# Kernel optimization log

Hardware: AMD Instinct MI355X
Metric: run time of the kernel (lower is better)

Reference implementation:

```python
import jax, jax.numpy as jnp
import numpy as np

D_MODEL = 1024
N_HEADS = 16
D_HEAD = D_MODEL // N_HEADS


def setup_inputs() -> dict:
    key = jax.random.key(0)
    ks = jax.random.split(key, 11)
    B, S = 2, 2048
    scale = 1.0 / np.sqrt(D_MODEL)
    inp = {
        "query": jax.random.normal(ks[0], (B, S, D_MODEL), jnp.float32),
        "key": jax.random.normal(ks[1], (B, S, D_MODEL), jnp.float32),
        "value": jax.random.normal(ks[2], (B, S, D_MODEL), jnp.float32),
        "Wq": jax.random.normal(ks[3], (D_MODEL, D_MODEL), jnp.float32) * scale,
        "bq": jnp.zeros((D_MODEL,), jnp.float32),
        "Wk": jax.random.normal(ks[4], (D_MODEL, D_MODEL), jnp.float32) * scale,
        "bk": jnp.zeros((D_MODEL,), jnp.float32),
        "Wv": jax.random.normal(ks[5], (D_MODEL, D_MODEL), jnp.float32) * scale,
        "bv": jnp.zeros((D_MODEL,), jnp.float32),
        "Wo": jax.random.normal(ks[6], (D_MODEL, D_MODEL), jnp.float32) * scale,
        "bo": jnp.zeros((D_MODEL,), jnp.float32),
    }
    return inp


def _split_heads(x):
    B, S, _ = x.shape
    return x.reshape(B, S, N_HEADS, D_HEAD).transpose(0, 2, 1, 3)  # [B,H,S,Dh]


def reference(query, key, value, Wq, bq, Wk, bk, Wv, bv, Wo, bo):
    q = _split_heads(query @ Wq + bq)
    k = _split_heads(key @ Wk + bk)
    v = _split_heads(value @ Wv + bv)
    # scores [B,H,S,S] -- faithfully materialized as in the original
    scores = jnp.einsum("bhqd,bhkd->bhqk", q, k) / np.sqrt(D_HEAD)
    attn = jax.nn.softmax(scores, axis=-1)
    out = jnp.einsum("bhqk,bhkd->bhqd", attn, v)  # [B,H,S,Dh]
    B, H, S, Dh = out.shape
    out = out.transpose(0, 2, 1, 3).reshape(B, S, H * Dh)
    return out @ Wo + bo
```

## Files before the change

kernel.cpp:

```cpp
#include <hip/hip_runtime.h>
#include <hip/hip_bf16.h>

using bf16 = __hip_bfloat16;
typedef __bf16 bf16x8 __attribute__((ext_vector_type(8)));
typedef __bf16 bf16x2v __attribute__((ext_vector_type(2)));
typedef float f32x4 __attribute__((ext_vector_type(4)));
typedef float f32x16 __attribute__((ext_vector_type(16)));

#define SEQ 2048
#define DM  1024
#define QSCALE 0.18033688011112042f

__device__ __forceinline__ f32x4 mfma16(bf16x8 a, bf16x8 b, f32x4 c) {
  return __builtin_amdgcn_mfma_f32_16x16x32_bf16(a, b, c, 0, 0, 0);
}
__device__ __forceinline__ f32x16 mfma32(bf16x8 a, bf16x8 b, f32x16 c) {
  return __builtin_amdgcn_mfma_f32_32x32x16_bf16(a, b, c, 0, 0, 0);
}
__device__ __forceinline__ void gload16(const void* g, void* l) {
  __builtin_amdgcn_global_load_lds(
      (const __attribute__((address_space(1))) unsigned int*)g,
      (__attribute__((address_space(3))) unsigned int*)l, 16, 0, 0);
}
__device__ __forceinline__ unsigned short bfbits(float x) {
  bf16 h = __float2bfloat16(x);
  return *reinterpret_cast<unsigned short*>(&h);
}
__device__ __forceinline__ unsigned pk2(float a, float b) {
#if __has_builtin(__builtin_amdgcn_cvt_pk_bf16_f32)
  bf16x2v r = __builtin_amdgcn_cvt_pk_bf16_f32(a, b);
  return *reinterpret_cast<unsigned*>(&r);
#else
  return (unsigned)bfbits(a) | ((unsigned)bfbits(b) << 16);
#endif
}
__device__ __forceinline__ float fexp2(float x) {
#if __has_builtin(__builtin_amdgcn_exp2f)
  return __builtin_amdgcn_exp2f(x);
#else
  return exp2f(x);
#endif
}
__device__ __forceinline__ void plswap(unsigned& a, unsigned& b) {
  asm("v_permlane32_swap_b32 %0, %1" : "+v"(a), "+v"(b));
}

__global__ __launch_bounds__(256) void cast_all(const float* __restrict__ q,
                                                const float* __restrict__ k,
                                                const float* __restrict__ v,
                                                const float* __restrict__ Wq,
                                                const float* __restrict__ Wk,
                                                const float* __restrict__ Wv,
                                                const float* __restrict__ Wo,
                                                bf16* __restrict__ Lx,
                                                bf16* __restrict__ Lw,
                                                bf16* __restrict__ Lwo) {
  __shared__ float tf[64][68];
  if (blockIdx.y < 3) {
    const float* src = blockIdx.y == 0 ? q : (blockIdx.y == 1 ? k : v);
    bf16* dst = Lx + (size_t)blockIdx.y * (4096ull * 1024) + (size_t)blockIdx.x * 16384;
#pragma unroll
    for (int i = 0; i < 8; ++i) {
      int u = threadIdx.x + i * 256;
      int k32 = u >> 6, l = u & 63;
      const float* p = src + (size_t)(blockIdx.x * 16 + (l & 15)) * 1024 + k32 * 32 + (l >> 4) * 8;
      float4 a = *(const float4*)p;
      float4 b = *(const float4*)(p + 4);
      alignas(16) unsigned o[4] = {pk2(a.x, a.y), pk2(a.z, a.w), pk2(b.x, b.y), pk2(b.z, b.w)};
      *(uint4*)(dst + (size_t)u * 8) = *(const uint4*)o;
    }
    return;
  }
  const int widx = blockIdx.y - 3;
  const float* W = widx == 0 ? Wq : (widx == 1 ? Wk : (widx == 2 ? Wv : Wo));
  bf16* dst = widx < 3 ? (Lw + (size_t)widx * 1048576) : Lwo;
  const int t = threadIdx.x, bx = blockIdx.x & 15, by = blockIdx.x >> 4;
#pragma unroll
  for (int i = 0; i < 4; ++i) {
    int u = t + i * 256, r = u >> 4, c4 = u & 15;
    *(float4*)&tf[r][c4 * 4] = *(const float4*)(W + (size_t)(by * 64 + r) * 1024 + bx * 64 + c4 * 4);
  }
  __syncthreads();
#pragma unroll
  for (int i = 0; i < 2; ++i) {
    int u = t + i * 256;
    int sub = u >> 6, l = u & 63;
    int n16l = sub >> 1, k32l = sub & 1;
    int nn = n16l * 16 + (l & 15);
    int kk = k32l * 32 + (l >> 4) * 8;
    alignas(16) unsigned o[4];
#pragma unroll
    for (int p = 0; p < 4; ++p) o[p] = pk2(tf[kk + 2 * p][nn], tf[kk + 2 * p + 1][nn]);
    size_t off = ((((size_t)(bx * 4 + n16l)) * 32 + (by * 2 + k32l)) * 64 + l) * 8;
    *(uint4*)(dst + off) = *(const uint4*)o;
  }
}

__global__ __launch_bounds__(512, 2) void qkv_gemm(const bf16* __restrict__ Lw,
                                                   const bf16* __restrict__ Lx,
                                                   const float* __restrict__ bq,
                                                   const float* __restrict__ bk,
                                                   const float* __restrict__ bv,
                                                   bf16* __restrict__ Lq,
                                                   bf16* __restrict__ Lk,
                                                   bf16* __restrict__ Lv) {
  __shared__ alignas(16) bf16 At[2][16384];
  __shared__ alignas(16) bf16 Bt[2][16384];
  const int t = threadIdx.x, lane = t & 63, w = t >> 6;
  const int m16 = lane & 15, g4 = lane >> 4;
  const int bid = blockIdx.y * 16 + blockIdx.x;
  const int logical = (bid & 7) * 24 + (bid >> 3);
  const int nt = logical & 15, ym = logical >> 4;
  const int third = ym >> 2, mt = ym & 3;
  const int wm = w >> 2, wn = w & 3;
  const bf16* Wb = Lw + (size_t)third * 1048576;
  const bf16* Xb = Lx + (size_t)third * (4096ull * 1024);
  f32x4 acc[8][4] = {};

#pragma unroll
  for (int ii = 0; ii < 4; ++ii) {
    int u = w * 4 + ii;
    gload16(Wb + (((size_t)(mt * 16 + (u >> 1)) * 32 + (u & 1)) * 64 + lane) * 8, (void*)&At[0][u * 512]);
    gload16(Xb + (((size_t)(nt * 16 + (u >> 1)) * 32 + (u & 1)) * 64 + lane) * 8, (void*)&Bt[0][u * 512]);
  }

  const bf16* Ab0 = (third < 2) ? At[0] : Bt[0];
  const bf16* Bb0 = (third < 2) ? Bt[0] : At[0];

  int cur = 0;
  for (int slab = 0; slab < 16; ++slab) {
    __builtin_amdgcn_s_barrier();
    __builtin_amdgcn_sched_barrier(0);
    if (slab < 15) {
      const int nb = cur ^ 1, k2 = (slab + 1) * 2;
#pragma unroll
      for (int ii = 0; ii < 4; ++ii) {
        int u = w * 4 + ii;
        gload16(Wb + (((size_t)(mt * 16 + (u >> 1)) * 32 + k2 + (u & 1)) * 64 + lane) * 8,
                (void*)&At[nb][u * 512]);
        gload16(Xb + (((size_t)(nt * 16 + (u >> 1)) * 32 + k2 + (u & 1)) * 64 + lane) * 8,
                (void*)&Bt[nb][u * 512]);
      }
      asm volatile("s_waitcnt vmcnt(8)" ::: "memory");
    } else {
      asm volatile("s_waitcnt vmcnt(0)" ::: "memory");
    }
    __builtin_amdgcn_sched_barrier(0);
    __builtin_amdgcn_s_barrier();
    __builtin_amdgcn_sched_barrier(0);

    const bf16* Ac = Ab0 + cur * 16384;
    const bf16* Bc = Bb0 + cur * 16384;
#pragma unroll
    for (int kc = 0; kc < 2; ++kc) {
      bf16x8 bfr[4];
#pragma unroll
      for (int nj = 0; nj < 4; ++nj)
        bfr[nj] = *(const bf16x8*)&Bc[((wn * 4 + nj) * 2 + kc) * 512 + lane * 8];
#pragma unroll
      for (int mh = 0; mh < 2; ++mh) {
        bf16x8 afr[4];
#pragma unroll
        for (int i = 0; i < 4; ++i)
          afr[i] = *(const bf16x8*)&Ac[((wm * 8 + mh * 4 + i) * 2 + kc) * 512 + lane * 8];
        __builtin_amdgcn_s_setprio(1);
#pragma unroll
        for (int i = 0; i < 4; ++i)
#pragma unroll
          for (int nj = 0; nj < 4; ++nj)
            acc[mh * 4 + i][nj] = mfma16(afr[i], bfr[nj], acc[mh * 4 + i][nj]);
        __builtin_amdgcn_s_setprio(0);
      }
    }
    cur ^= 1;
  }

  if (third < 2) {
    bf16* dst = third == 0 ? Lq : Lk;
    const float* bias = third == 0 ? bq : bk;
    const float sc = third == 0 ? QSCALE : 1.0f;
#pragma unroll
    for (int mi = 0; mi < 8; ++mi) {
      int doutb = mt * 256 + wm * 128 + mi * 16 + g4 * 4;
      float4 b4 = *(const float4*)(bias + doutb);
      int hh = doutb >> 6, d32 = (doutb & 63) >> 5;
      int lhi = (doutb & 31) >> 3, half = g4 & 1;
#pragma unroll
      for (int nj = 0; nj < 4; ++nj) {
        int seq = nt * 256 + wn * 64 + nj * 16 + m16;
        int bb2 = seq >> 11, s16w = (seq & 2047) >> 4;
        size_t off = ((((size_t)(bb2 * 128 + s16w)) * 16 + hh) * 2 + d32) * 512 + (m16 + 16 * lhi) * 8 + half * 4;
        uint2 pv;
        pv.x = pk2((acc[mi][nj][0] + b4.x) * sc, (acc[mi][nj][1] + b4.y) * sc);
        pv.y = pk2((acc[mi][nj][2] + b4.z) * sc, (acc[mi][nj][3] + b4.w) * sc);
        *(uint2*)(dst + off) = pv;
      }
    }
  } else {
#pragma unroll
    for (int nj = 0; nj < 4; ++nj) {
      int dout = mt * 256 + wn * 64 + nj * 16 + m16;
      float bvv = bv[dout];
      int hh = dout >> 6, dt = (dout & 63) >> 4;
#pragma unroll
      for (int mi = 0; mi < 8; ++mi) {
        int seqb = nt * 256 + wm * 128 + mi * 16 + g4 * 4;
        int b_ = seqb >> 11, kt = (seqb & 2047) >> 6, ks32 = (seqb & 63) >> 5;
        int lhi = (seqb & 31) >> 3, half = g4 & 1;
        size_t off = (((((size_t)(b_ * 32 + kt)) * 16 + hh) * 4 + dt) * 2 + ks32) * 512 + (m16 + 16 * lhi) * 8 + half * 4;
        uint2 pv;
        pv.x = pk2(acc[mi][nj][0] + bvv, acc[mi][nj][1] + bvv);
        pv.y = pk2(acc[mi][nj][2] + bvv, acc[mi][nj][3] + bvv);
        *(uint2*)(Lv + off) = pv;
      }
    }
  }
}

__global__ __launch_bounds__(512, 4) void flash(const bf16* __restrict__ Lq,
                                                const bf16* __restrict__ Lk,
                                                const bf16* __restrict__ Lv,
                                                bf16* __restrict__ Lab) {
  __shared__ alignas(16) unsigned char smem[65536];
  bf16* const Kb = (bf16*)smem;
  bf16* const Vb = (bf16*)(smem + 32768);

  const int t = threadIdx.x, lane = t & 63, w = t >> 6;
  const int l31 = lane & 31, m16 = lane & 15, hi = lane >> 5, b4 = (lane >> 4) & 1;
  const int qw = w >> 1, g = w & 1, wg = w >> 1;
  const int bid = blockIdx.x;
  const int logical = ((bid & 7) << 6) | (bid >> 3);
  const int qt = logical & 15, h = (logical >> 4) & 15, b = logical >> 8;

  bf16x8 qf[4];
  {
    const int sQ = b * 128 + qt * 8 + qw * 2 + b4;
#pragma unroll
    for (int ks = 0; ks < 4; ++ks) {
      const int d32 = ks >> 1, g4q = (ks & 1) * 2 + hi;
      qf[ks] = *(const bf16x8*)(Lq + (((size_t)sQ * 16 + h) * 2 + d32) * 512 + (m16 + 16 * g4q) * 8);
    }
  }

  const int ss = wg >> 1, sd = wg & 1;
#pragma unroll
  for (int u = 0; u < 2; ++u) {
    const bf16* gk = Lk + ((((size_t)(b * 128 + g * 64 + u * 2 + ss)) * 16 + h) * 2 + sd) * 512 + lane * 8;
    gload16(gk, (void*)(Kb + (g * 2 + 0) * 4096 + u * 2048 + wg * 512));
    const bf16* gv = Lv + (((((size_t)(b * 32 + g * 16)) * 16 + h) * 4 + wg) * 2 + u) * 512 + lane * 8;
    gload16(gv, (void*)(Vb + (g * 2 + 0) * 4096 + u * 2048 + wg * 512));
  }

  float lrow = 0.f;
  f32x16 oacc[2] = {};
  __syncthreads();

  for (int it = 0; it < 16; ++it) {
    const int cur = it & 1;
    const bf16* const Klb = Kb + (g * 2 + cur) * 4096;
    const bf16* const Vlb = Vb + (g * 2 + cur) * 4096;
    if (it < 15) {
      const int nb = cur ^ 1;
#pragma unroll
      for (int u = 0; u < 2; ++u) {
        const int kc = (it + 1) * 2 + u;
        const bf16* gk = Lk + ((((size_t)(b * 128 + g * 64 + kc * 2 + ss)) * 16 + h) * 2 + sd) * 512 + lane * 8;
        gload16(gk, (void*)(Kb + (g * 2 + nb) * 4096 + u * 2048 + wg * 512));
        const bf16* gv = Lv + (((((size_t)(b * 32 + g * 16 + (kc >> 1))) * 16 + h) * 4 + wg) * 2 + (kc & 1)) * 512 + lane * 8;
        gload16(gv, (void*)(Vb + (g * 2 + nb) * 4096 + u * 2048 + wg * 512));
      }
    }

#pragma unroll
    for (int u = 0; u < 2; ++u) {
      const bf16* const Kl = Klb + u * 2048;
      const bf16* const Vl = Vlb + u * 2048;

      f32x16 s = {};
      __builtin_amdgcn_s_setprio(1);
#pragma unroll
      for (int ks = 0; ks < 4; ++ks) {
        const int d32 = ks >> 1, g4k = (ks & 1) * 2 + hi;
        bf16x8 kf = *(const bf16x8*)&Kl[((b4 * 2 + d32) * 64 + m16 + 16 * g4k) * 8];
        s = mfma32(kf, qf[ks], s);
      }
      __builtin_amdgcn_s_setprio(0);

      float e[16];
#pragma unroll
      for (int r = 0; r < 16; ++r) e[r] = fexp2(s[r]);
      {
        float a0 = e[0] + e[1], a1 = e[2] + e[3], a2 = e[4] + e[5], a3 = e[6] + e[7];
        float a4 = e[8] + e[9], a5 = e[10] + e[11], a6 = e[12] + e[13], a7 = e[14] + e[15];
        lrow += ((a0 + a1) + (a2 + a3)) + ((a4 + a5) + (a6 + a7));
      }
      bf16x8 bP[2];
#pragma unroll
      for (int c = 0; c < 2; ++c) {
        unsigned P0 = pk2(e[8 * c + 0], e[8 * c + 1]);
        unsigned P1 = pk2(e[8 * c + 2], e[8 * c + 3]);
        unsigned P2 = pk2(e[8 * c + 4], e[8 * c + 5]);
        unsigned P3 = pk2(e[8 * c + 6], e[8 * c + 7]);
        plswap(P0, P2);
        plswap(P1, P3);
        alignas(16) unsigned pw[4] = {P0, P1, P2, P3};
        bP[c] = *(const bf16x8*)pw;
      }

      __builtin_amdgcn_s_setprio(1);
#pragma unroll
      for (int dtile = 0; dtile < 2; ++dtile) {
        const int dt = dtile * 2 + b4;
#pragma unroll
        for (int c = 0; c < 2; ++c) {
          bf16x8 av = *(const bf16x8*)&Vl[(dt * 64 + m16 + 16 * (2 * c + hi)) * 8];
          oacc[dtile] = mfma32(av, bP[c], oacc[dtile]);
        }
      }
      __builtin_amdgcn_s_setprio(0);
    }
    __syncthreads();
  }

  lrow += __shfl_xor(lrow, 32);

  float* const Os = (float*)smem;
  float* const Ls = (float*)(smem + 32768);
  if (g == 1) {
#pragma unroll
    for (int dtile = 0; dtile < 2; ++dtile)
#pragma unroll
      for (int r = 0; r < 16; ++r)
        Os[((qw * 2 + dtile) * 16 + r) * 64 + lane] = oacc[dtile][r];
    if (hi == 0) Ls[qw * 32 + l31] = lrow;
  }
  __syncthreads();
  if (g == 0) {
    const float inv = 1.f / (lrow + Ls[qw * 32 + l31]);
    const int sQ = b * 128 + qt * 8 + qw * 2 + b4;
#pragma unroll
    for (int dtile = 0; dtile < 2; ++dtile) {
      const int k32 = h * 2 + dtile;
#pragma unroll
      for (int j = 0; j < 8; ++j) {
        const int r = 2 * j;
        float o0 = oacc[dtile][r] + Os[((qw * 2 + dtile) * 16 + r) * 64 + lane];
        float o1 = oacc[dtile][r + 1] + Os[((qw * 2 + dtile) * 16 + r + 1) * 64 + lane];
        unsigned pv = pk2(o0 * inv, o1 * inv);
        size_t off = ((size_t)sQ * 32 + k32) * 512 + (m16 + 16 * (r >> 2)) * 8 + 4 * hi + (r & 3);
        *(unsigned*)(Lab + off) = pv;
      }
    }
  }
}

__global__ __launch_bounds__(256) void out_gemm(const bf16* __restrict__ Lab,
                                                const bf16* __restrict__ Lwo,
                                                const float* __restrict__ bo,
                                                float* __restrict__ out) {
  __shared__ alignas(16) bf16 Al[2][8192];
  __shared__ alignas(16) bf16 Bl[2][4096];
  const int t = threadIdx.x, lane = t & 63, w = t >> 6;
  const int m16 = lane & 15, g4 = lane >> 4;
  const int bid = blockIdx.y * 16 + blockIdx.x;
  const int logical = (bid & 7) * 64 + (bid >> 3);
  const int nt = logical & 15, mt = logical >> 4;
  const int wm = w >> 1, wn = w & 1;
  f32x4 acc[4][2] = {};

#pragma unroll
  for (int ii = 0; ii < 4; ++ii) {
    int s = w * 4 + ii;
    gload16(Lab + (((size_t)(mt * 8 + (s >> 1))) * 32 + (s & 1)) * 512 + lane * 8, (void*)&Al[0][s * 512]);
  }
#pragma unroll
  for (int ii = 0; ii < 2; ++ii) {
    int s = w * 2 + ii;
    gload16(Lwo + (((size_t)(nt * 4 + (s >> 1))) * 32 + (s & 1)) * 512 + lane * 8, (void*)&Bl[0][s * 512]);
  }

  int cur = 0;
  for (int slab = 0; slab < 16; ++slab) {
    __builtin_amdgcn_s_barrier();
    __builtin_amdgcn_sched_barrier(0);
    if (slab < 15) {
      const int nb = cur ^ 1, ns = slab + 1;
#pragma unroll
      for (int ii = 0; ii < 4; ++ii) {
        int s = w * 4 + ii;
        gload16(Lab + (((size_t)(mt * 8 + (s >> 1))) * 32 + ns * 2 + (s & 1)) * 512 + lane * 8,
                (void*)&Al[nb][s * 512]);
      }
#pragma unroll
      for (int ii = 0; ii < 2; ++ii) {
        int s = w * 2 + ii;
        gload16(Lwo + (((size_t)(nt * 4 + (s >> 1))) * 32 + ns * 2 + (s & 1)) * 512 + lane * 8,
                (void*)&Bl[nb][s * 512]);
      }
      asm volatile("s_waitcnt vmcnt(6)" ::: "memory");
    } else {
      asm volatile("s_waitcnt vmcnt(0)" ::: "memory");
    }
    __builtin_amdgcn_sched_barrier(0);
    __builtin_amdgcn_s_barrier();
    __builtin_amdgcn_sched_barrier(0);
#pragma unroll
    for (int c = 0; c < 2; ++c) {
      bf16x8 aA[4], bW[2];
#pragma unroll
      for (int i = 0; i < 4; ++i) aA[i] = *(const bf16x8*)&Al[cur][((wm * 4 + i) * 2 + c) * 512 + lane * 8];
#pragma unroll
      for (int j = 0; j < 2; ++j) bW[j] = *(const bf16x8*)&Bl[cur][((wn * 2 + j) * 2 + c) * 512 + lane * 8];
      __builtin_amdgcn_s_setprio(1);
#pragma unroll
      for (int i = 0; i < 4; ++i)
#pragma unroll
        for (int j = 0; j < 2; ++j) acc[i][j] = mfma16(aA[i], bW[j], acc[i][j]);
      __builtin_amdgcn_s_setprio(0);
    }
    cur ^= 1;
  }
#pragma unroll
  for (int j = 0; j < 2; ++j) {
    int n = nt * 64 + wn * 32 + j * 16 + m16;
    float bb = bo[n];
#pragma unroll
    for (int i = 0; i < 4; ++i) {
      int seqb = mt * 128 + wm * 64 + i * 16 + g4 * 4;
#pragma unroll
      for (int r = 0; r < 4; ++r) out[(size_t)(seqb + r) * 1024 + n] = acc[i][j][r] + bb;
    }
  }
}

extern "C" void kernel_launch(void* const* d_in, const int* in_sizes, int n_in,
                              void* d_out, int out_size, void* d_ws, size_t ws_size,
                              hipStream_t stream) {
  const float* query = (const float*)d_in[0];
  const float* key   = (const float*)d_in[1];
  const float* value = (const float*)d_in[2];
  const float* Wq = (const float*)d_in[3];
  const float* bq = (const float*)d_in[4];
  const float* Wk = (const float*)d_in[5];
  const float* bk = (const float*)d_in[6];
  const float* Wv = (const float*)d_in[7];
  const float* bv = (const float*)d_in[8];
  const float* Wo = (const float*)d_in[9];
  const float* bo = (const float*)d_in[10];
  float* out = (float*)d_out;

  bf16* Lw  = (bf16*)d_ws;
  bf16* Lwo = Lw + 3ull * 1048576;
  bf16* Lx  = Lwo + 1048576;
  bf16* Lq  = Lx + 3ull * 4194304;
  bf16* Lk  = Lq + 4194304;
  bf16* Lv  = Lk + 4194304;
  bf16* Lab = Lv + 4194304;

  cast_all<<<dim3(256, 7), 256, 0, stream>>>(query, key, value, Wq, Wk, Wv, Wo, Lx, Lw, Lwo);
  qkv_gemm<<<dim3(16, 12), 512, 0, stream>>>(Lw, Lx, bq, bk, bv, Lq, Lk, Lv);
  flash<<<512, 512, 0, stream>>>(Lq, Lk, Lv, Lab);
  out_gemm<<<dim3(16, 32), 256, 0, stream>>>(Lab, Lwo, bo, out);
}
```

Baseline: 215.8 us.

## Load K/V fragments directly from global memory in flash kernel, dropping LDS staging

Removes the double-buffered LDS staging of K and V tiles in the flash attention kernel. Each wave now reads its K and V MFMA fragments straight from the pre-swizzled global layout, which removes the per-iteration block barrier. Shared memory shrinks to the final reduction buffers and the launch bound occupancy hint rises from 4 to 6. The cost is that fragments shared across waves are fetched redundantly through the cache hierarchy, and global load latency is exposed to the MFMA chain with no explicit prefetch.

```diff
diff --git a/kernel.cpp b/kernel.cpp
--- a/kernel.cpp
+++ b/kernel.cpp
@@ -217,17 +217,16 @@
   }
 }
 
-__global__ __launch_bounds__(512, 4) void flash(const bf16* __restrict__ Lq,
+__global__ __launch_bounds__(512, 6) void flash(const bf16* __restrict__ Lq,
                                                 const bf16* __restrict__ Lk,
                                                 const bf16* __restrict__ Lv,
                                                 bf16* __restrict__ Lab) {
-  __shared__ alignas(16) unsigned char smem[65536];
-  bf16* const Kb = (bf16*)smem;
-  bf16* const Vb = (bf16*)(smem + 32768);
+  __shared__ alignas(16) float Os[8 * 16 * 64];
+  __shared__ float Ls[4 * 32];
 
   const int t = threadIdx.x, lane = t & 63, w = t >> 6;
   const int l31 = lane & 31, m16 = lane & 15, hi = lane >> 5, b4 = (lane >> 4) & 1;
-  const int qw = w >> 1, g = w & 1, wg = w >> 1;
+  const int qw = w >> 1, g = w & 1;
   const int bid = blockIdx.x;
   const int logical = ((bid & 7) << 6) | (bid >> 3);
   const int qt = logical & 15, h = (logical >> 4) & 15, b = logical >> 8;
@@ -242,49 +241,29 @@
     }
   }
 
-  const int ss = wg >> 1, sd = wg & 1;
-#pragma unroll
-  for (int u = 0; u < 2; ++u) {
-    const bf16* gk = Lk + ((((size_t)(b * 128 + g * 64 + u * 2 + ss)) * 16 + h) * 2 + sd) * 512 + lane * 8;
-    gload16(gk, (void*)(Kb + (g * 2 + 0) * 4096 + u * 2048 + wg * 512));
-    const bf16* gv = Lv + (((((size_t)(b * 32 + g * 16)) * 16 + h) * 4 + wg) * 2 + u) * 512 + lane * 8;
-    gload16(gv, (void*)(Vb + (g * 2 + 0) * 4096 + u * 2048 + wg * 512));
-  }
-
   float lrow = 0.f;
   f32x16 oacc[2] = {};
-  __syncthreads();
 
   for (int it = 0; it < 16; ++it) {
-    const int cur = it & 1;
-    const bf16* const Klb = Kb + (g * 2 + cur) * 4096;
-    const bf16* const Vlb = Vb + (g * 2 + cur) * 4096;
-    if (it < 15) {
-      const int nb = cur ^ 1;
-#pragma unroll
-      for (int u = 0; u < 2; ++u) {
-        const int kc = (it + 1) * 2 + u;
-        const bf16* gk = Lk + ((((size_t)(b * 128 + g * 64 + kc * 2 + ss)) * 16 + h) * 2 + sd) * 512 + lane * 8;
-        gload16(gk, (void*)(Kb + (g * 2 + nb) * 4096 + u * 2048 + wg * 512));
-        const bf16* gv = Lv + (((((size_t)(b * 32 + g * 16 + (kc >> 1))) * 16 + h) * 4 + wg) * 2 + (kc & 1)) * 512 + lane * 8;
-        gload16(gv, (void*)(Vb + (g * 2 + nb) * 4096 + u * 2048 + wg * 512));
-      }
-    }
-
 #pragma unroll
     for (int u = 0; u < 2; ++u) {
-      const bf16* const Kl = Klb + u * 2048;
-      const bf16* const Vl = Vlb + u * 2048;
+      const int kc2 = it * 2 + u;
 
       f32x16 s = {};
-      __builtin_amdgcn_s_setprio(1);
-#pragma unroll
-      for (int ks = 0; ks < 4; ++ks) {
-        const int d32 = ks >> 1, g4k = (ks & 1) * 2 + hi;
-        bf16x8 kf = *(const bf16x8*)&Kl[((b4 * 2 + d32) * 64 + m16 + 16 * g4k) * 8];
-        s = mfma32(kf, qf[ks], s);
-      }
-      __builtin_amdgcn_s_setprio(0);
+      {
+        bf16x8 kf[4];
+#pragma unroll
+        for (int ks = 0; ks < 4; ++ks) {
+          const int d32 = ks >> 1, g4k = (ks & 1) * 2 + hi;
+          kf[ks] = *(const bf16x8*)(Lk +
+              ((((size_t)(b * 128 + g * 64 + kc2 * 2 + b4)) * 16 + h) * 2 + d32) * 512 +
+              (m16 + 16 * g4k) * 8);
+        }
+        __builtin_amdgcn_s_setprio(1);
+#pragma unroll
+        for (int ks = 0; ks < 4; ++ks) s = mfma32(kf[ks], qf[ks], s);
+        __builtin_amdgcn_s_setprio(0);
+      }
 
       float e[16];
 #pragma unroll
@@ -307,25 +286,22 @@
         bP[c] = *(const bf16x8*)pw;
       }
 
+      const size_t vb = ((((size_t)(b * 32 + g * 16 + (kc2 >> 1))) * 16 + h) * 4) * 2 + (kc2 & 1);
       __builtin_amdgcn_s_setprio(1);
 #pragma unroll
       for (int dtile = 0; dtile < 2; ++dtile) {
         const int dt = dtile * 2 + b4;
-#pragma unroll
-        for (int c = 0; c < 2; ++c) {
-          bf16x8 av = *(const bf16x8*)&Vl[(dt * 64 + m16 + 16 * (2 * c + hi)) * 8];
-          oacc[dtile] = mfma32(av, bP[c], oacc[dtile]);
-        }
+        bf16x8 av0 = *(const bf16x8*)(Lv + (vb + dt * 2) * 512 + (m16 + 16 * hi) * 8);
+        bf16x8 av1 = *(const bf16x8*)(Lv + (vb + dt * 2) * 512 + (m16 + 16 * (2 + hi)) * 8);
+        oacc[dtile] = mfma32(av0, bP[0], oacc[dtile]);
+        oacc[dtile] = mfma32(av1, bP[1], oacc[dtile]);
       }
       __builtin_amdgcn_s_setprio(0);
     }
-    __syncthreads();
   }
 
   lrow += __shfl_xor(lrow, 32);
 
-  float* const Os = (float*)smem;
-  float* const Ls = (float*)(smem + 32768);
   if (g == 1) {
 #pragma unroll
     for (int dtile = 0; dtile < 2; ++dtile)
```

Result: slower. 260.4 us (+20.7%).

## Shrink QKV GEMM tile to 256x128 with single-k32 slabs and 384 blocks

Applied to the files above, without the earlier changes.

Reworks the fused QKV projection GEMM to use 256x128 output tiles instead of 256x256, loading one 32-wide k slice per stage (32 iterations) instead of two. The grid grows from 192 to 384 blocks, with less shared memory and fewer accumulators per block, so more blocks can be resident (launch bounds raised to 4) and the 256 CUs are better filled. In exchange, operand reuse per tile drops, raising global and LDS traffic per FLOP, and the shallower per-iteration work gives the double-buffered pipeline less time to hide load latency.

```diff
diff --git a/kernel.cpp b/kernel.cpp
--- a/kernel.cpp
+++ b/kernel.cpp
@@ -96,7 +96,7 @@
   }
 }
 
-__global__ __launch_bounds__(512, 2) void qkv_gemm(const bf16* __restrict__ Lw,
+__global__ __launch_bounds__(512, 4) void qkv_gemm(const bf16* __restrict__ Lw,
                                                    const bf16* __restrict__ Lx,
                                                    const float* __restrict__ bq,
                                                    const float* __restrict__ bk,
@@ -104,44 +104,48 @@
                                                    bf16* __restrict__ Lq,
                                                    bf16* __restrict__ Lk,
                                                    bf16* __restrict__ Lv) {
-  __shared__ alignas(16) bf16 At[2][16384];
-  __shared__ alignas(16) bf16 Bt[2][16384];
+  __shared__ alignas(16) bf16 At[2][8192];
+  __shared__ alignas(16) bf16 Bt[2][4096];
   const int t = threadIdx.x, lane = t & 63, w = t >> 6;
   const int m16 = lane & 15, g4 = lane >> 4;
-  const int bid = blockIdx.y * 16 + blockIdx.x;
-  const int logical = (bid & 7) * 24 + (bid >> 3);
-  const int nt = logical & 15, ym = logical >> 4;
-  const int third = ym >> 2, mt = ym & 3;
-  const int wm = w >> 2, wn = w & 3;
+  const int bid = blockIdx.x;
+  const int logical = (bid & 7) * 48 + (bid >> 3);
+  const int third = logical >> 7;
+  const int r = logical & 127;
+  const int shift = third < 2 ? 5 : 3;
+  const int mt = r >> shift, nt = r & ((1 << shift) - 1);
+  const int wm = w >> 1, wn = w & 1;
   const bf16* Wb = Lw + (size_t)third * 1048576;
   const bf16* Xb = Lx + (size_t)third * (4096ull * 1024);
-  f32x4 acc[8][4] = {};
-
-#pragma unroll
-  for (int ii = 0; ii < 4; ++ii) {
-    int u = w * 4 + ii;
-    gload16(Wb + (((size_t)(mt * 16 + (u >> 1)) * 32 + (u & 1)) * 64 + lane) * 8, (void*)&At[0][u * 512]);
-    gload16(Xb + (((size_t)(nt * 16 + (u >> 1)) * 32 + (u & 1)) * 64 + lane) * 8, (void*)&Bt[0][u * 512]);
-  }
-
-  const bf16* Ab0 = (third < 2) ? At[0] : Bt[0];
-  const bf16* Bb0 = (third < 2) ? Bt[0] : At[0];
+  const bf16* Asrc = third < 2 ? Wb : Xb;
+  const bf16* Bsrc = third < 2 ? Xb : Wb;
+  f32x4 acc[4][4] = {};
+
+#pragma unroll
+  for (int ii = 0; ii < 3; ++ii) {
+    int u = w * 3 + ii;
+    if (u < 16)
+      gload16(Asrc + (((size_t)(mt * 16 + u) * 32 + 0) * 64 + lane) * 8, (void*)&At[0][u * 512]);
+    else
+      gload16(Bsrc + (((size_t)(nt * 8 + u - 16) * 32 + 0) * 64 + lane) * 8, (void*)&Bt[0][(u - 16) * 512]);
+  }
 
   int cur = 0;
-  for (int slab = 0; slab < 16; ++slab) {
+  for (int k = 0; k < 32; ++k) {
     __builtin_amdgcn_s_barrier();
     __builtin_amdgcn_sched_barrier(0);
-    if (slab < 15) {
-      const int nb = cur ^ 1, k2 = (slab + 1) * 2;
-#pragma unroll
-      for (int ii = 0; ii < 4; ++ii) {
-        int u = w * 4 + ii;
-        gload16(Wb + (((size_t)(mt * 16 + (u >> 1)) * 32 + k2 + (u & 1)) * 64 + lane) * 8,
-                (void*)&At[nb][u * 512]);
-        gload16(Xb + (((size_t)(nt * 16 + (u >> 1)) * 32 + k2 + (u & 1)) * 64 + lane) * 8,
-                (void*)&Bt[nb][u * 512]);
-      }
-      asm volatile("s_waitcnt vmcnt(8)" ::: "memory");
+    if (k < 31) {
+      const int nb = cur ^ 1;
+#pragma unroll
+      for (int ii = 0; ii < 3; ++ii) {
+        int u = w * 3 + ii;
+        if (u < 16)
+          gload16(Asrc + (((size_t)(mt * 16 + u) * 32 + k + 1) * 64 + lane) * 8, (void*)&At[nb][u * 512]);
+        else
+          gload16(Bsrc + (((size_t)(nt * 8 + u - 16) * 32 + k + 1) * 64 + lane) * 8,
+                  (void*)&Bt[nb][(u - 16) * 512]);
+      }
+      asm volatile("s_waitcnt vmcnt(3)" ::: "memory");
     } else {
       asm volatile("s_waitcnt vmcnt(0)" ::: "memory");
     }
@@ -149,29 +153,17 @@
     __builtin_amdgcn_s_barrier();
     __builtin_amdgcn_sched_barrier(0);
 
-    const bf16* Ac = Ab0 + cur * 16384;
-    const bf16* Bc = Bb0 + cur * 16384;
-#pragma unroll
-    for (int kc = 0; kc < 2; ++kc) {
-      bf16x8 bfr[4];
-#pragma unroll
-      for (int nj = 0; nj < 4; ++nj)
-        bfr[nj] = *(const bf16x8*)&Bc[((wn * 4 + nj) * 2 + kc) * 512 + lane * 8];
-#pragma unroll
-      for (int mh = 0; mh < 2; ++mh) {
-        bf16x8 afr[4];
-#pragma unroll
-        for (int i = 0; i < 4; ++i)
-          afr[i] = *(const bf16x8*)&Ac[((wm * 8 + mh * 4 + i) * 2 + kc) * 512 + lane * 8];
-        __builtin_amdgcn_s_setprio(1);
-#pragma unroll
-        for (int i = 0; i < 4; ++i)
-#pragma unroll
-          for (int nj = 0; nj < 4; ++nj)
-            acc[mh * 4 + i][nj] = mfma16(afr[i], bfr[nj], acc[mh * 4 + i][nj]);
-        __builtin_amdgcn_s_setprio(0);
-      }
-    }
+    bf16x8 afr[4], bfr[4];
+#pragma unroll
+    for (int i = 0; i < 4; ++i) afr[i] = *(const bf16x8*)&At[cur][(wm * 4 + i) * 512 + lane * 8];
+#pragma unroll
+    for (int j = 0; j < 4; ++j) bfr[j] = *(const bf16x8*)&Bt[cur][(wn * 4 + j) * 512 + lane * 8];
+    __builtin_amdgcn_s_setprio(1);
+#pragma unroll
+    for (int i = 0; i < 4; ++i)
+#pragma unroll
+      for (int j = 0; j < 4; ++j) acc[i][j] = mfma16(afr[i], bfr[j], acc[i][j]);
+    __builtin_amdgcn_s_setprio(0);
     cur ^= 1;
   }
 
@@ -180,14 +172,14 @@
     const float* bias = third == 0 ? bq : bk;
     const float sc = third == 0 ? QSCALE : 1.0f;
 #pragma unroll
-    for (int mi = 0; mi < 8; ++mi) {
-      int doutb = mt * 256 + wm * 128 + mi * 16 + g4 * 4;
+    for (int mi = 0; mi < 4; ++mi) {
+      int doutb = mt * 256 + wm * 64 + mi * 16 + g4 * 4;
       float4 b4 = *(const float4*)(bias + doutb);
       int hh = doutb >> 6, d32 = (doutb & 63) >> 5;
       int lhi = (doutb & 31) >> 3, half = g4 & 1;
 #pragma unroll
       for (int nj = 0; nj < 4; ++nj) {
-        int seq = nt * 256 + wn * 64 + nj * 16 + m16;
+        int seq = nt * 128 + wn * 64 + nj * 16 + m16;
         int bb2 = seq >> 11, s16w = (seq & 2047) >> 4;
         size_t off = ((((size_t)(bb2 * 128 + s16w)) * 16 + hh) * 2 + d32) * 512 + (m16 + 16 * lhi) * 8 + half * 4;
         uint2 pv;
@@ -199,12 +191,12 @@
   } else {
 #pragma unroll
     for (int nj = 0; nj < 4; ++nj) {
-      int dout = mt * 256 + wn * 64 + nj * 16 + m16;
+      int dout = nt * 128 + wn * 64 + nj * 16 + m16;
       float bvv = bv[dout];
       int hh = dout >> 6, dt = (dout & 63) >> 4;
 #pragma unroll
-      for (int mi = 0; mi < 8; ++mi) {
-        int seqb = nt * 256 + wm * 128 + mi * 16 + g4 * 4;
+      for (int mi = 0; mi < 4; ++mi) {
+        int seqb = mt * 256 + wm * 64 + mi * 16 + g4 * 4;
         int b_ = seqb >> 11, kt = (seqb & 2047) >> 6, ks32 = (seqb & 63) >> 5;
         int lhi = (seqb & 31) >> 3, half = g4 & 1;
         size_t off = (((((size_t)(b_ * 32 + kt)) * 16 + hh) * 4 + dt) * 2 + ks32) * 512 + (m16 + 16 * lhi) * 8 + half * 4;
@@ -458,7 +450,7 @@
   bf16* Lab = Lv + 4194304;
 
   cast_all<<<dim3(256, 7), 256, 0, stream>>>(query, key, value, Wq, Wk, Wv, Wo, Lx, Lw, Lwo);
-  qkv_gemm<<<dim3(16, 12), 512, 0, stream>>>(Lw, Lx, bq, bk, bv, Lq, Lk, Lv);
+  qkv_gemm<<<384, 512, 0, stream>>>(Lw, Lx, bq, bk, bv, Lq, Lk, Lv);
   flash<<<512, 512, 0, stream>>>(Lq, Lk, Lv, Lab);
   out_gemm<<<dim3(16, 32), 256, 0, stream>>>(Lab, Lwo, bo, out);
 }
```

Result: faster. 210.4 us (-2.5%).
